# Kernel optimization log

Measured on AMD Instinct MI355X. Metric: run time of the kernel, lower is better.

Reference implementation:

```python
import jax, jax.numpy as jnp
import numpy as np

# --- hyperparameters (from MambaBlock init) ---
DIM = 256          # d_model per window
STEP = 128         # int(dim * hop), hop = 0.5
N_MAMBA = 2
D_STATE = 16
D_CONV = 4
EXPAND = 4
D_INNER = EXPAND * DIM          # 1024
DT_RANK = -(-DIM // 16)         # ceil(d_model/16) = 16
EPS = 1e-5
B_SZ = 4
T_LEN = 131072


def setup_inputs() -> dict:
    key = jax.random.key(0)
    ks = jax.random.split(key, 8)
    s = 0.02
    x = jax.random.normal(ks[0], (B_SZ, T_LEN), dtype=jnp.float32)
    in_proj_w = jax.random.normal(ks[1], (N_MAMBA, 2 * D_INNER, DIM), dtype=jnp.float32) * s
    conv_w = jax.random.normal(ks[2], (N_MAMBA, D_INNER, 1, D_CONV), dtype=jnp.float32) * 0.1
    conv_b = jnp.zeros((N_MAMBA, D_INNER), dtype=jnp.float32)
    x_proj_w = jax.random.normal(ks[3], (N_MAMBA, DT_RANK + 2 * D_STATE, D_INNER), dtype=jnp.float32) * s
    dt_std = DT_RANK ** -0.5
    dt_proj_w = jax.random.uniform(ks[4], (N_MAMBA, D_INNER, DT_RANK), minval=-dt_std, maxval=dt_std, dtype=jnp.float32)
    # dt bias: inverse-softplus of dt ~ LogUniform[1e-3, 0.1] (mamba_ssm init)
    dt = jnp.exp(jax.random.uniform(ks[5], (N_MAMBA, D_INNER), dtype=jnp.float32)
                 * (np.log(0.1) - np.log(1e-3)) + np.log(1e-3))
    dt_proj_b = dt + jnp.log(-jnp.expm1(-dt))
    A_log = jnp.log(jnp.broadcast_to(jnp.arange(1, D_STATE + 1, dtype=jnp.float32),
                                     (N_MAMBA, D_INNER, D_STATE)))
    D_param = jnp.ones((N_MAMBA, D_INNER), dtype=jnp.float32)
    out_proj_w = jax.random.normal(ks[6], (N_MAMBA, DIM, D_INNER), dtype=jnp.float32) * s
    norm_w = jnp.ones((N_MAMBA, DIM), dtype=jnp.float32)
    return dict(x=x, in_proj_w=in_proj_w, conv_w=conv_w, conv_b=conv_b,
                x_proj_w=x_proj_w, dt_proj_w=dt_proj_w, dt_proj_b=dt_proj_b,
                A_log=A_log, D_param=D_param, out_proj_w=out_proj_w, norm_w=norm_w)


def _rmsnorm(x, w):
    return x * jax.lax.rsqrt(jnp.mean(x * x, axis=-1, keepdims=True) + EPS) * w


def _selective_scan(u, delta, A, Bm, Cm, Dp):
    # u, delta: [B, L, Di]; A: [Di, N]; Bm, Cm: [B, L, N]; Dp: [Di]
    def step(h, inp):
        u_t, d_t, B_t, C_t = inp                       # [B,Di],[B,Di],[B,N],[B,N]
        dA = jnp.exp(d_t[:, :, None] * A)              # [B,Di,N]
        h = dA * h + (d_t * u_t)[:, :, None] * B_t[:, None, :]
        y_t = jnp.einsum('bdn,bn->bd', h, C_t)
        return h, y_t
    h0 = jnp.zeros((u.shape[0], u.shape[2], A.shape[1]), u.dtype)
    xs = (u.transpose(1, 0, 2), delta.transpose(1, 0, 2),
          Bm.transpose(1, 0, 2), Cm.transpose(1, 0, 2))
    _, ys = jax.lax.scan(step, h0, xs)                 # ys: [L, B, Di]
    return ys.transpose(1, 0, 2) + u * Dp


def _mamba(x, in_w, cw, cb, xp_w, dt_w, dt_b, A_log, Dp, out_w):
    # x: [B, L, d_model]
    xz = jnp.einsum('bld,ed->ble', x, in_w)            # [B, L, 2*Di]
    xc, z = jnp.split(xz, 2, axis=-1)
    # causal depthwise conv (torch pads d_conv-1 both sides then truncates to L)
    xc = xc.transpose(0, 2, 1)                         # [B, Di, L]
    xc = jax.lax.conv_general_dilated(xc, cw, window_strides=(1,),
                                      padding=[(D_CONV - 1, 0)],
                                      feature_group_count=D_INNER,
                                      dimension_numbers=('NCH', 'OIH', 'NCH'))
    xc = jax.nn.silu(xc + cb[None, :, None]).transpose(0, 2, 1)  # [B, L, Di]
    x_dbl = jnp.einsum('bld,ed->ble', xc, xp_w)        # [B, L, dt_rank + 2N]
    dt = x_dbl[..., :DT_RANK]
    Bm = x_dbl[..., DT_RANK:DT_RANK + D_STATE]
    Cm = x_dbl[..., DT_RANK + D_STATE:]
    delta = jax.nn.softplus(jnp.einsum('blr,dr->bld', dt, dt_w) + dt_b)
    A = -jnp.exp(A_log)                                # [Di, N]
    y = _selective_scan(xc, delta, A, Bm, Cm, Dp)
    y = y * jax.nn.silu(z)
    return jnp.einsum('bld,ed->ble', y, out_w)         # [B, L, d_model]


def _forward(x, in_proj_w, conv_w, conv_b, x_proj_w, dt_proj_w, dt_proj_b,
             A_log, D_param, out_proj_w, norm_w):
    B, T = x.shape
    L = (T - DIM) // STEP + 1
    idx = jnp.arange(L)[:, None] * STEP + jnp.arange(DIM)[None, :]  # [L, DIM]
    h = x[:, idx]                                      # unfold -> [B, L, DIM]
    res = None
    for i in range(N_MAMBA):
        res = h + res if res is not None else h        # Block residual chaining
        hn = _rmsnorm(res, norm_w[i])
        h = _mamba(hn, in_proj_w[i], conv_w[i], conv_b[i], x_proj_w[i],
                   dt_proj_w[i], dt_proj_b[i], A_log[i], D_param[i], out_proj_w[i])
    r = h + res
    # hop < 1: triangular window, then fold (overlap-add)
    half = DIM // 2
    win = jnp.concatenate([jnp.linspace(0.0, 1.0, half), jnp.linspace(1.0, 0.0, half)])
    r = r * win
    folded = jnp.zeros_like(x).at[:, idx].add(r)       # F.fold overlap-add
    return folded + x


def reference(x, in_proj_w, conv_w, conv_b, x_proj_w, dt_proj_w, dt_proj_b,
              A_log, D_param, out_proj_w, norm_w):
    return _forward(x, in_proj_w, conv_w, conv_b, x_proj_w, dt_proj_w, dt_proj_b,
                    A_log, D_param, out_proj_w, norm_w)
```

## Files before the change

### kernel.cpp

```cpp
#include <hip/hip_runtime.h>
#include <cmath>

#define DIMC   256
#define L_WIN  1023
#define M_VALID 4092
#define M_PAD  4096
#define DI     1024
#define TLEN   131072
#define SEG    64
#define NSEG   16

typedef __bf16 bf16x8 __attribute__((ext_vector_type(8)));
typedef __bf16 bf16x4 __attribute__((ext_vector_type(4)));
typedef float  f32x4  __attribute__((ext_vector_type(4)));

__device__ __forceinline__ float sigmoidf_(float x){ return 1.f/(1.f + __expf(-x)); }
__device__ __forceinline__ float softplusf_(float v){ return fmaxf(v,0.f) + log1pf(__expf(-fabsf(v))); }

template<int CTRL>
__device__ __forceinline__ float dpp_add(float x){
  int v = __builtin_amdgcn_update_dpp(0, __builtin_bit_cast(int, x), CTRL, 0xF, 0xF, true);
  return x + __builtin_bit_cast(float, v);
}

__global__ void cvt_bf16_kernel(const float* __restrict__ s, __bf16* __restrict__ d, int n){
  int i = blockIdx.x*256 + threadIdx.x;
  int stride = gridDim.x*256;
  for (; i < n; i += stride) d[i] = (__bf16)s[i];
}

__global__ __launch_bounds__(256) void frame_kernel(const float* __restrict__ x, float* __restrict__ res){
  int m = blockIdx.x, j = threadIdx.x;
  float v = 0.f;
  if (m < M_VALID){
    int b = m / L_WIN, l = m - b*L_WIN;
    v = x[(size_t)b*TLEN + l*128 + j];
  }
  res[(size_t)m*DIMC + j] = v;
}

__global__ __launch_bounds__(256) void rms_kernel(const float* __restrict__ src, __bf16* __restrict__ dst,
                                                  const float* __restrict__ w){
  int m = blockIdx.x, j = threadIdx.x;
  float v = (m < M_VALID) ? src[(size_t)m*DIMC + j] : 0.f;
  float s = v*v;
  #pragma unroll
  for (int off = 32; off; off >>= 1) s += __shfl_down(s, off);
  __shared__ float ls[4];
  if ((threadIdx.x & 63) == 0) ls[threadIdx.x >> 6] = s;
  __syncthreads();
  float tot = ls[0] + ls[1] + ls[2] + ls[3];
  float scale = rsqrtf(tot * (1.f/DIMC) + 1e-5f);
  dst[(size_t)m*DIMC + j] = (__bf16)(v * scale * w[j]);
}

template<int WM, int WN, typename OutT>
__global__ __launch_bounds__(256) void gemm_tiled_kernel(const __bf16* __restrict__ A, const __bf16* __restrict__ B,
    OutT* C, const float* addsrc, int K, int ldc)
{
  constexpr int BM  = 32*WM;
  constexpr int BN  = 32*WN;
  constexpr int LDK = 72;
  __shared__ __bf16 As[BM*LDK];
  __shared__ __bf16 Bs[BN*LDK];
  int tid  = threadIdx.x;
  int lane = tid & 63, wv = tid >> 6;
  int row  = lane & 15, kq = lane >> 4;
  int m0 = blockIdx.x*BM, n0 = blockIdx.y*BN;
  int wmo = (wv >> 1)*(16*WM);
  int wno = (wv &  1)*(16*WN);
  f32x4 acc[WM][WN] = {};
  for (int kt = 0; kt < K; kt += 64){
    __syncthreads();
    #pragma unroll
    for (int r = 0; r < BM/32; ++r){
      int seg = r*256 + tid;
      int rw = seg >> 3, sb = seg & 7;
      *(bf16x8*)(As + rw*LDK + sb*8) = *(const bf16x8*)(A + (size_t)(m0 + rw)*K + kt + sb*8);
    }
    #pragma unroll
    for (int r = 0; r < BN/32; ++r){
      int seg = r*256 + tid;
      int rw = seg >> 3, sb = seg & 7;
      *(bf16x8*)(Bs + rw*LDK + sb*8) = *(const bf16x8*)(B + (size_t)(n0 + rw)*K + kt + sb*8);
    }
    __syncthreads();
    #pragma unroll
    for (int ks = 0; ks < 2; ++ks){
      bf16x8 af[WM], bfr[WN];
      #pragma unroll
      for (int i = 0; i < WM; ++i) af[i]  = *(const bf16x8*)(As + (wmo + i*16 + row)*LDK + ks*32 + kq*8);
      #pragma unroll
      for (int j = 0; j < WN; ++j) bfr[j] = *(const bf16x8*)(Bs + (wno + j*16 + row)*LDK + ks*32 + kq*8);
      #pragma unroll
      for (int i = 0; i < WM; ++i){
        #pragma unroll
        for (int j = 0; j < WN; ++j)
          acc[i][j] = __builtin_amdgcn_mfma_f32_16x16x32_bf16(af[i], bfr[j], acc[i][j], 0, 0, 0);
      }
    }
  }
  #pragma unroll
  for (int i = 0; i < WM; ++i){
    int cm = m0 + wmo + i*16 + kq*4;
    #pragma unroll
    for (int j = 0; j < WN; ++j){
      int cn = n0 + wno + j*16 + row;
      #pragma unroll
      for (int ii = 0; ii < 4; ++ii){
        size_t idx = (size_t)(cm + ii)*ldc + cn;
        float v = acc[i][j][ii];
        if (addsrc) v += addsrc[idx];
        C[idx] = (OutT)v;
      }
    }
  }
}

template<int SUBN, typename OutT>
__global__ __launch_bounds__(256) void gemm_kernel(const __bf16* __restrict__ A, const __bf16* __restrict__ B,
    OutT* C, const float* addsrc, int K, int ldc)
{
  int lane = threadIdx.x & 63;
  int wv   = threadIdx.x >> 6;
  int row  = lane & 15;
  int kq   = lane >> 4;
  int m0 = blockIdx.x*64 + wv*16;
  int n0 = blockIdx.y*(16*SUBN);
  f32x4 acc[SUBN] = {};
  const __bf16* Ap = A + (size_t)(m0 + row)*K + kq*8;
  const __bf16* Bp = B + (size_t)(n0 + row)*K + kq*8;
  for (int k = 0; k < K; k += 32){
    bf16x8 a = *(const bf16x8*)(Ap + k);
    #pragma unroll
    for (int s = 0; s < SUBN; ++s){
      bf16x8 bb = *(const bf16x8*)(Bp + (size_t)s*16*K + k);
      acc[s] = __builtin_amdgcn_mfma_f32_16x16x32_bf16(a, bb, acc[s], 0, 0, 0);
    }
  }
  int cm = m0 + kq*4;
  #pragma unroll
  for (int s = 0; s < SUBN; ++s){
    int cn = n0 + s*16 + row;
    #pragma unroll
    for (int i = 0; i < 4; ++i){
      size_t idx = (size_t)(cm + i)*ldc + cn;
      float v = acc[s][i];
      if (addsrc) v += addsrc[idx];
      C[idx] = (OutT)v;
    }
  }
}

__global__ __launch_bounds__(256) void conv_kernel(const __bf16* __restrict__ xz16, const float* __restrict__ cw,
    const float* __restrict__ cb, __bf16* __restrict__ u16)
{
  int m0 = blockIdx.x * 16;
  int d  = threadIdx.x * 4;
  float w[4][4];
  #pragma unroll
  for (int c = 0; c < 4; ++c){
    #pragma unroll
    for (int j = 0; j < 4; ++j) w[c][j] = cw[(d + c)*4 + j];
  }
  float bias[4];
  #pragma unroll
  for (int c = 0; c < 4; ++c) bias[c] = cb[d + c];
  for (int ti = 0; ti < 16; ++ti){
    int m = m0 + ti;
    float acc[4] = {0.f, 0.f, 0.f, 0.f};
    if (m < M_VALID){
      int b = m / L_WIN;
      int l = m - b*L_WIN;
      #pragma unroll
      for (int c = 0; c < 4; ++c) acc[c] = bias[c];
      #pragma unroll
      for (int k = 0; k < 4; ++k){
        if (l >= k){
          bf16x4 xv = *(const bf16x4*)(xz16 + (size_t)(m - k)*2048 + d);
          #pragma unroll
          for (int c = 0; c < 4; ++c) acc[c] = fmaf((float)xv[c], w[c][3-k], acc[c]);
        }
      }
      #pragma unroll
      for (int c = 0; c < 4; ++c) acc[c] = acc[c] * sigmoidf_(acc[c]);
    }
    bf16x4 o;
    #pragma unroll
    for (int c = 0; c < 4; ++c) o[c] = (__bf16)acc[c];
    *(bf16x4*)(u16 + (size_t)m*DI + d) = o;
  }
}

__global__ __launch_bounds__(256) void dtproj_kernel(const float* __restrict__ xdbl, const float* __restrict__ dtw,
    const float* __restrict__ dtb, __bf16* __restrict__ delta16)
{
  int m0 = blockIdx.x * 16;
  int tid = threadIdx.x;
  __shared__ float sdt[16][17];
  sdt[tid >> 4][tid & 15] = xdbl[(size_t)(m0 + (tid >> 4))*48 + (tid & 15)];
  __syncthreads();
  int d0 = tid * 4;
  float w[4][16];
  #pragma unroll
  for (int c = 0; c < 4; ++c){
    #pragma unroll
    for (int q = 0; q < 16; ++q) w[c][q] = dtw[(d0 + c)*16 + q];
  }
  float bias[4];
  #pragma unroll
  for (int c = 0; c < 4; ++c) bias[c] = dtb[d0 + c];
  for (int t = 0; t < 16; ++t){
    float acc[4] = {bias[0], bias[1], bias[2], bias[3]};
    #pragma unroll
    for (int r = 0; r < 16; ++r){
      float dv = sdt[t][r];
      #pragma unroll
      for (int c = 0; c < 4; ++c) acc[c] = fmaf(dv, w[c][r], acc[c]);
    }
    bf16x4 o;
    #pragma unroll
    for (int c = 0; c < 4; ++c) o[c] = (__bf16)softplusf_(acc[c]);
    *(bf16x4*)(delta16 + (size_t)(m0 + t)*DI + d0) = o;
  }
}

__global__ __launch_bounds__(256) void scan_part1_kernel(
  const __bf16* __restrict__ u16, const __bf16* __restrict__ delta16,
  const float* __restrict__ xdbl, const float* __restrict__ Alog, float2* __restrict__ Pq)
{
  int bid = blockIdx.x;
  int s = bid & 15, dtile = (bid >> 4) & 63, b = bid >> 10;
  int d0 = dtile << 4;
  int tid = threadIdx.x;
  int c = tid >> 4, n = tid & 15;
  float A_dn = -__expf(Alog[(d0 + c)*16 + n]);
  __shared__ float2 sdd[16][SEG+2];
  __shared__ float  sB [SEG][17];
  int t0 = s*SEG;
  int nt = L_WIN - t0; if (nt > SEG) nt = SEG;
  size_t base_m = (size_t)b*L_WIN + t0;
  for (int i2 = tid; i2 < 16*SEG; i2 += 256){
    int tt = i2 >> 4, dd = i2 & 15;
    float dlt = 0.f, du = 0.f, Bv = 0.f;
    if (tt < nt){
      size_t m = base_m + tt;
      dlt = (float)delta16[m*DI + d0 + dd];
      du  = dlt * (float)u16[m*DI + d0 + dd];
      Bv  = xdbl[m*48 + 16 + dd];
    }
    sdd[dd][tt] = make_float2(dlt, du);
    sB[tt][dd]  = Bv;
  }
  __syncthreads();
  float h = 0.f, P = 1.f;
  #pragma unroll 8
  for (int t = 0; t < SEG; ++t){
    float2 dd2 = sdd[c][t];
    float dA = __expf(dd2.x * A_dn);
    h = fmaf(dA, h, dd2.y * sB[t][n]);
    P *= dA;
  }
  Pq[(((size_t)b*NSEG + s) << 14) + d0*16 + tid] = make_float2(P, h);
}

__global__ __launch_bounds__(256) void scan_combine_kernel(const float2* __restrict__ Pq,
                                                           float* __restrict__ hstart)
{
  int idx = blockIdx.x*256 + threadIdx.x;
  int b = idx >> 14;
  int dn = idx & 16383;
  float hs = 0.f;
  #pragma unroll
  for (int s = 0; s < NSEG; ++s){
    size_t o = (((size_t)b*NSEG + s) << 14) + dn;
    hstart[o] = hs;
    float2 pq = Pq[o];
    hs = fmaf(pq.x, hs, pq.y);
  }
}

__global__ __launch_bounds__(256) void scan_part2_kernel(
  const __bf16* __restrict__ u16, const __bf16* __restrict__ delta16,
  const float* __restrict__ xdbl, const __bf16* __restrict__ xz16,
  const float* __restrict__ Alog, const float* __restrict__ Dp,
  const float* __restrict__ hstart, __bf16* __restrict__ y16)
{
  int bid = blockIdx.x;
  int s = bid & 15, dtile = (bid >> 4) & 63, b = bid >> 10;
  int d0 = dtile << 4;
  int tid = threadIdx.x;
  int c = tid >> 4, n = tid & 15;
  float A_dn = -__expf(Alog[(d0 + c)*16 + n]);
  __shared__ float2 sdd[16][SEG+2];
  __shared__ float2 sBC[SEG][17];
  __shared__ float  sy [16][SEG+1];
  __shared__ float  sD[16];
  if (tid < 16) sD[tid] = Dp[d0 + tid];
  int t0 = s*SEG;
  int nt = L_WIN - t0; if (nt > SEG) nt = SEG;
  size_t base_m = (size_t)b*L_WIN + t0;
  for (int i2 = tid; i2 < 16*SEG; i2 += 256){
    int tt = i2 >> 4, dd = i2 & 15;
    float dlt = 0.f, du = 0.f, Bv = 0.f, Cv = 0.f;
    if (tt < nt){
      size_t m = base_m + tt;
      dlt = (float)delta16[m*DI + d0 + dd];
      du  = dlt * (float)u16[m*DI + d0 + dd];
      Bv  = xdbl[m*48 + 16 + dd];
      Cv  = xdbl[m*48 + 32 + dd];
    }
    sdd[dd][tt] = make_float2(dlt, du);
    sBC[tt][dd] = make_float2(Bv, Cv);
  }
  float h = hstart[(((size_t)b*NSEG + s) << 14) + d0*16 + tid];
  __syncthreads();
  #pragma unroll 8
  for (int t = 0; t < SEG; ++t){
    float2 dd2 = sdd[c][t];
    float dA = __expf(dd2.x * A_dn);
    float2 bc = sBC[t][n];
    h = fmaf(dA, h, dd2.y * bc.x);
    float pp = h * bc.y;
    pp = dpp_add<0xB1>(pp);
    pp = dpp_add<0x4E>(pp);
    pp = dpp_add<0x141>(pp);
    pp = dpp_add<0x128>(pp);
    if (n == 0) sy[c][t] = pp;
  }
  __syncthreads();
  for (int i2 = tid; i2 < 16*nt; i2 += 256){
    int tt = i2 >> 4, dd = i2 & 15;
    size_t m = base_m + tt;
    float uv = (float)u16[m*DI + d0 + dd];
    float zv = (float)xz16[m*2048 + 1024 + d0 + dd];
    float yv = (sy[dd][tt] + uv * sD[dd]) * (zv * sigmoidf_(zv));
    y16[m*DI + d0 + dd] = (__bf16)yv;
  }
}

__global__ __launch_bounds__(256) void fold_kernel(const float* __restrict__ x, const float* __restrict__ r,
                                                   float* __restrict__ out){
  int i = blockIdx.x*256 + threadIdx.x;
  int b = i >> 17;
  int t = i & (TLEN - 1);
  float acc = x[i];
  int l1 = t >> 7;
  int j  = t & 127;
  if (l1 < L_WIN) acc += r[((size_t)b*L_WIN + l1)*DIMC + j] * ((float)j * (1.f/127.f));
  if (l1 >= 1)    acc += r[((size_t)b*L_WIN + l1 - 1)*DIMC + j + 128] * ((float)(127 - j) * (1.f/127.f));
  out[i] = acc;
}

extern "C" void kernel_launch(void* const* d_in, const int* in_sizes, int n_in,
                              void* d_out, int out_size, void* d_ws, size_t ws_size,
                              hipStream_t stream)
{
  (void)in_sizes; (void)n_in; (void)out_size; (void)ws_size;
  const float* x      = (const float*)d_in[0];
  const float* in_w   = (const float*)d_in[1];
  const float* conv_w = (const float*)d_in[2];
  const float* conv_b = (const float*)d_in[3];
  const float* xp_w   = (const float*)d_in[4];
  const float* dt_w   = (const float*)d_in[5];
  const float* dt_b   = (const float*)d_in[6];
  const float* A_log  = (const float*)d_in[7];
  const float* Dp     = (const float*)d_in[8];
  const float* out_w  = (const float*)d_in[9];
  const float* norm_w = (const float*)d_in[10];
  float* out = (float*)d_out;

  char* p = (char*)d_ws;
  auto alloc = [&](size_t bytes)->void*{ void* r = (void*)p; p += (bytes + 255) & ~(size_t)255; return r; };
  float*  res    = (float*) alloc((size_t)M_PAD*DIMC*4);
  __bf16* hn16   = (__bf16*)alloc((size_t)M_PAD*DIMC*2);
  __bf16* xz16   = (__bf16*)alloc((size_t)M_PAD*2048*2);
  __bf16* u16    = (__bf16*)alloc((size_t)M_PAD*DI*2);
  float*  xdbl   = (float*) alloc((size_t)M_PAD*48*4);
  __bf16* delta16= (__bf16*)alloc((size_t)M_PAD*DI*2);
  __bf16* y16    = (__bf16*)alloc((size_t)M_PAD*DI*2);
  float2* Pq     = (float2*)alloc((size_t)4*NSEG*16384*8);
  float*  hstart = (float*) alloc((size_t)4*NSEG*16384*4);
  __bf16* w_in16 = (__bf16*)alloc((size_t)2*2048*256*2);
  __bf16* w_xp16 = (__bf16*)alloc((size_t)2*48*1024*2);
  __bf16* w_out16= (__bf16*)alloc((size_t)2*256*1024*2);

  cvt_bf16_kernel<<<512, 256, 0, stream>>>(in_w,  w_in16,  2*2048*256);
  cvt_bf16_kernel<<<128, 256, 0, stream>>>(xp_w,  w_xp16,  2*48*1024);
  cvt_bf16_kernel<<<256, 256, 0, stream>>>(out_w, w_out16, 2*256*1024);
  frame_kernel<<<M_PAD, 256, 0, stream>>>(x, res);

  for (int i = 0; i < 2; ++i){
    rms_kernel<<<M_PAD, 256, 0, stream>>>(res, hn16, norm_w + i*256);
    gemm_tiled_kernel<4, 4, __bf16><<<dim3(32, 16), 256, 0, stream>>>(hn16, w_in16 + (size_t)i*524288, xz16, nullptr, 256, 2048);
    conv_kernel<<<M_PAD/16, 256, 0, stream>>>(xz16, conv_w + i*4096, conv_b + i*1024, u16);
    gemm_kernel<1, float><<<dim3(64, 3), 256, 0, stream>>>(u16, w_xp16 + (size_t)i*49152, xdbl, nullptr, 1024, 48);
    dtproj_kernel<<<M_PAD/16, 256, 0, stream>>>(xdbl, dt_w + i*16384, dt_b + i*1024, delta16);
    scan_part1_kernel<<<4096, 256, 0, stream>>>(u16, delta16, xdbl, A_log + i*16384, Pq);
    scan_combine_kernel<<<256, 256, 0, stream>>>(Pq, hstart);
    scan_part2_kernel<<<4096, 256, 0, stream>>>(u16, delta16, xdbl, xz16, A_log + i*16384, Dp + i*1024,
                                                hstart, y16);
    gemm_tiled_kernel<2, 2, float><<<dim3(64, 4), 256, 0, stream>>>(y16, w_out16 + (size_t)i*262144, res, res, 1024, 256);
  }
  fold_kernel<<<TLEN*4/256, 256, 0, stream>>>(x, res, out);
}
```

Baseline: 359.5 us.

## Fold scan combine into part2, vectorize scan loads, use exp2 and partial DPP reduce

Removes the separate scan_combine kernel: each scan_part2 block now computes its own starting state by serially combining the preceding segment summaries from Pq, which drops one launch and the hstart buffer. Shared-memory staging is rewritten to use vector loads of bf16x4 delta/u and float4 B/C with a time-major layout. The exponential switches to the hardware exp2 with a pre-scaled A. The C·h reduction uses only two DPP steps, storing four bf16 partial sums per channel that are summed in the epilogue. The epilogue is vectorized as well. The trade-offs are redundant prefix work in later segments, extra rounding from keeping the partial sums in bf16, and possible shared-memory bank conflicts from the new layout.

```diff
diff --git a/kernel.cpp b/kernel.cpp
--- a/kernel.cpp
+++ b/kernel.cpp
@@ -14,8 +14,18 @@
 typedef __bf16 bf16x4 __attribute__((ext_vector_type(4)));
 typedef float  f32x4  __attribute__((ext_vector_type(4)));
 
+#define LOG2E 1.4426950408889634f
+
 __device__ __forceinline__ float sigmoidf_(float x){ return 1.f/(1.f + __expf(-x)); }
 __device__ __forceinline__ float softplusf_(float v){ return fmaxf(v,0.f) + log1pf(__expf(-fabsf(v))); }
+
+__device__ __forceinline__ float fast_exp2(float x){
+#if __has_builtin(__builtin_amdgcn_exp2f)
+  return __builtin_amdgcn_exp2f(x);
+#else
+  return __expf(x * 0.6931471805599453f);
+#endif
+}
 
 template<int CTRL>
 __device__ __forceinline__ float dpp_add(float x){
@@ -234,108 +244,117 @@
   int d0 = dtile << 4;
   int tid = threadIdx.x;
   int c = tid >> 4, n = tid & 15;
-  float A_dn = -__expf(Alog[(d0 + c)*16 + n]);
-  __shared__ float2 sdd[16][SEG+2];
-  __shared__ float  sB [SEG][17];
+  float A2 = -__expf(Alog[(d0 + c)*16 + n]) * LOG2E;
+  __shared__ float2 sdd[SEG][16];
+  __shared__ float  sB [SEG][16];
   int t0 = s*SEG;
   int nt = L_WIN - t0; if (nt > SEG) nt = SEG;
   size_t base_m = (size_t)b*L_WIN + t0;
-  for (int i2 = tid; i2 < 16*SEG; i2 += 256){
-    int tt = i2 >> 4, dd = i2 & 15;
-    float dlt = 0.f, du = 0.f, Bv = 0.f;
+  {
+    int tt = tid >> 2, dq = tid & 3;
+    f32x4 lo = {0,0,0,0}, hi = {0,0,0,0}, B4 = {0,0,0,0};
     if (tt < nt){
       size_t m = base_m + tt;
-      dlt = (float)delta16[m*DI + d0 + dd];
-      du  = dlt * (float)u16[m*DI + d0 + dd];
-      Bv  = xdbl[m*48 + 16 + dd];
-    }
-    sdd[dd][tt] = make_float2(dlt, du);
-    sB[tt][dd]  = Bv;
+      bf16x4 dl4 = *(const bf16x4*)(delta16 + m*DI + d0 + dq*4);
+      bf16x4 uu4 = *(const bf16x4*)(u16     + m*DI + d0 + dq*4);
+      B4 = *(const f32x4*)(xdbl + m*48 + 16 + dq*4);
+      lo = f32x4{(float)dl4[0], (float)dl4[0]*(float)uu4[0], (float)dl4[1], (float)dl4[1]*(float)uu4[1]};
+      hi = f32x4{(float)dl4[2], (float)dl4[2]*(float)uu4[2], (float)dl4[3], (float)dl4[3]*(float)uu4[3]};
+    }
+    f32x4* p0 = (f32x4*)&sdd[tt][dq*4];
+    p0[0] = lo; p0[1] = hi;
+    *(f32x4*)&sB[tt][dq*4] = B4;
   }
   __syncthreads();
   float h = 0.f, P = 1.f;
   #pragma unroll 8
   for (int t = 0; t < SEG; ++t){
-    float2 dd2 = sdd[c][t];
-    float dA = __expf(dd2.x * A_dn);
+    float2 dd2 = sdd[t][c];
+    float dA = fast_exp2(dd2.x * A2);
     h = fmaf(dA, h, dd2.y * sB[t][n]);
     P *= dA;
   }
   Pq[(((size_t)b*NSEG + s) << 14) + d0*16 + tid] = make_float2(P, h);
-}
-
-__global__ __launch_bounds__(256) void scan_combine_kernel(const float2* __restrict__ Pq,
-                                                           float* __restrict__ hstart)
-{
-  int idx = blockIdx.x*256 + threadIdx.x;
-  int b = idx >> 14;
-  int dn = idx & 16383;
-  float hs = 0.f;
-  #pragma unroll
-  for (int s = 0; s < NSEG; ++s){
-    size_t o = (((size_t)b*NSEG + s) << 14) + dn;
-    hstart[o] = hs;
-    float2 pq = Pq[o];
-    hs = fmaf(pq.x, hs, pq.y);
-  }
 }
 
 __global__ __launch_bounds__(256) void scan_part2_kernel(
   const __bf16* __restrict__ u16, const __bf16* __restrict__ delta16,
   const float* __restrict__ xdbl, const __bf16* __restrict__ xz16,
   const float* __restrict__ Alog, const float* __restrict__ Dp,
-  const float* __restrict__ hstart, __bf16* __restrict__ y16)
+  const float2* __restrict__ Pq, __bf16* __restrict__ y16)
 {
   int bid = blockIdx.x;
   int s = bid & 15, dtile = (bid >> 4) & 63, b = bid >> 10;
   int d0 = dtile << 4;
   int tid = threadIdx.x;
   int c = tid >> 4, n = tid & 15;
-  float A_dn = -__expf(Alog[(d0 + c)*16 + n]);
-  __shared__ float2 sdd[16][SEG+2];
-  __shared__ float2 sBC[SEG][17];
-  __shared__ float  sy [16][SEG+1];
+  float A2 = -__expf(Alog[(d0 + c)*16 + n]) * LOG2E;
+  __shared__ float2 sdd[SEG][16];
+  __shared__ float2 sBC[SEG][16];
+  __shared__ __bf16 sy4[16][SEG][4];
   __shared__ float  sD[16];
   if (tid < 16) sD[tid] = Dp[d0 + tid];
   int t0 = s*SEG;
   int nt = L_WIN - t0; if (nt > SEG) nt = SEG;
   size_t base_m = (size_t)b*L_WIN + t0;
-  for (int i2 = tid; i2 < 16*SEG; i2 += 256){
-    int tt = i2 >> 4, dd = i2 & 15;
-    float dlt = 0.f, du = 0.f, Bv = 0.f, Cv = 0.f;
+  {
+    int tt = tid >> 2, dq = tid & 3;
+    f32x4 lo = {0,0,0,0}, hi = {0,0,0,0}, bc0 = {0,0,0,0}, bc1 = {0,0,0,0};
     if (tt < nt){
       size_t m = base_m + tt;
-      dlt = (float)delta16[m*DI + d0 + dd];
-      du  = dlt * (float)u16[m*DI + d0 + dd];
-      Bv  = xdbl[m*48 + 16 + dd];
-      Cv  = xdbl[m*48 + 32 + dd];
-    }
-    sdd[dd][tt] = make_float2(dlt, du);
-    sBC[tt][dd] = make_float2(Bv, Cv);
-  }
-  float h = hstart[(((size_t)b*NSEG + s) << 14) + d0*16 + tid];
+      bf16x4 dl4 = *(const bf16x4*)(delta16 + m*DI + d0 + dq*4);
+      bf16x4 uu4 = *(const bf16x4*)(u16     + m*DI + d0 + dq*4);
+      f32x4 B4 = *(const f32x4*)(xdbl + m*48 + 16 + dq*4);
+      f32x4 C4 = *(const f32x4*)(xdbl + m*48 + 32 + dq*4);
+      lo = f32x4{(float)dl4[0], (float)dl4[0]*(float)uu4[0], (float)dl4[1], (float)dl4[1]*(float)uu4[1]};
+      hi = f32x4{(float)dl4[2], (float)dl4[2]*(float)uu4[2], (float)dl4[3], (float)dl4[3]*(float)uu4[3]};
+      bc0 = f32x4{B4[0], C4[0], B4[1], C4[1]};
+      bc1 = f32x4{B4[2], C4[2], B4[3], C4[3]};
+    }
+    f32x4* p0 = (f32x4*)&sdd[tt][dq*4];
+    p0[0] = lo; p0[1] = hi;
+    f32x4* p1 = (f32x4*)&sBC[tt][dq*4];
+    p1[0] = bc0; p1[1] = bc1;
+  }
+  float h = 0.f;
+  {
+    const float2* pqb = Pq + (((size_t)b*NSEG) << 14) + d0*16 + tid;
+    for (int k = 0; k < s; ++k){
+      float2 pq = pqb[(size_t)k << 14];
+      h = fmaf(pq.x, h, pq.y);
+    }
+  }
   __syncthreads();
   #pragma unroll 8
   for (int t = 0; t < SEG; ++t){
-    float2 dd2 = sdd[c][t];
-    float dA = __expf(dd2.x * A_dn);
+    float2 dd2 = sdd[t][c];
+    float dA = fast_exp2(dd2.x * A2);
     float2 bc = sBC[t][n];
     h = fmaf(dA, h, dd2.y * bc.x);
     float pp = h * bc.y;
     pp = dpp_add<0xB1>(pp);
     pp = dpp_add<0x4E>(pp);
-    pp = dpp_add<0x141>(pp);
-    pp = dpp_add<0x128>(pp);
-    if (n == 0) sy[c][t] = pp;
+    if ((n & 3) == 0) sy4[c][t][n >> 2] = (__bf16)pp;
   }
   __syncthreads();
-  for (int i2 = tid; i2 < 16*nt; i2 += 256){
-    int tt = i2 >> 4, dd = i2 & 15;
-    size_t m = base_m + tt;
-    float uv = (float)u16[m*DI + d0 + dd];
-    float zv = (float)xz16[m*2048 + 1024 + d0 + dd];
-    float yv = (sy[dd][tt] + uv * sD[dd]) * (zv * sigmoidf_(zv));
-    y16[m*DI + d0 + dd] = (__bf16)yv;
+  {
+    int tt = tid >> 2, dq = tid & 3;
+    if (tt < nt){
+      size_t m = base_m + tt;
+      bf16x4 uv4 = *(const bf16x4*)(u16  + m*DI   + d0 + dq*4);
+      bf16x4 zv4 = *(const bf16x4*)(xz16 + m*2048 + 1024 + d0 + dq*4);
+      bf16x4 o;
+      #pragma unroll
+      for (int c2 = 0; c2 < 4; ++c2){
+        int dd = dq*4 + c2;
+        bf16x4 p4 = *(const bf16x4*)&sy4[dd][tt][0];
+        float yv = ((float)p4[0] + (float)p4[1]) + ((float)p4[2] + (float)p4[3]);
+        float zv = (float)zv4[c2];
+        yv = (yv + (float)uv4[c2] * sD[dd]) * (zv * sigmoidf_(zv));
+        o[c2] = (__bf16)yv;
+      }
+      *(bf16x4*)(y16 + m*DI + d0 + dq*4) = o;
+    }
   }
 }
 
@@ -380,7 +399,6 @@
   __bf16* delta16= (__bf16*)alloc((size_t)M_PAD*DI*2);
   __bf16* y16    = (__bf16*)alloc((size_t)M_PAD*DI*2);
   float2* Pq     = (float2*)alloc((size_t)4*NSEG*16384*8);
-  float*  hstart = (float*) alloc((size_t)4*NSEG*16384*4);
   __bf16* w_in16 = (__bf16*)alloc((size_t)2*2048*256*2);
   __bf16* w_xp16 = (__bf16*)alloc((size_t)2*48*1024*2);
   __bf16* w_out16= (__bf16*)alloc((size_t)2*256*1024*2);
@@ -397,9 +415,8 @@
     gemm_kernel<1, float><<<dim3(64, 3), 256, 0, stream>>>(u16, w_xp16 + (size_t)i*49152, xdbl, nullptr, 1024, 48);
     dtproj_kernel<<<M_PAD/16, 256, 0, stream>>>(xdbl, dt_w + i*16384, dt_b + i*1024, delta16);
     scan_part1_kernel<<<4096, 256, 0, stream>>>(u16, delta16, xdbl, A_log + i*16384, Pq);
-    scan_combine_kernel<<<256, 256, 0, stream>>>(Pq, hstart);
     scan_part2_kernel<<<4096, 256, 0, stream>>>(u16, delta16, xdbl, xz16, A_log + i*16384, Dp + i*1024,
-                                                hstart, y16);
+                                                Pq, y16);
     gemm_tiled_kernel<2, 2, float><<<dim3(64, 4), 256, 0, stream>>>(y16, w_out16 + (size_t)i*262144, res, res, 1024, 256);
   }
   fold_kernel<<<TLEN*4/256, 256, 0, stream>>>(x, res, out);
```

Result: slower. 367.9 us (+2.3%).
